# Kernel optimization log

Hardware: AMD Instinct MI355X
Metric: run time of the kernel (lower is better)

## Reference

```python
import math
import jax, jax.numpy as jnp
import numpy as np

EPS = 1e-8
N_ITER = 5


def _partial_ot(C, reg):
    # C: (M, N) cost matrix. Faithful to partial_optimal_transport with
    # diag-matmuls replaced by equivalent broadcast row/col scaling.
    M, N = C.shape
    a = jnp.full((M,), 1.0 / M, dtype=C.dtype)
    b = jnp.full((N,), 1.0 / N, dtype=C.dtype)
    m = jnp.minimum(a.sum(), b.sum())  # = 1.0 here
    K = jnp.exp(-C / jnp.clip(reg, EPS))
    K = K * (m / jnp.clip(K.sum(), EPS))

    def body(K, _):
        r = jnp.minimum(a / jnp.clip(K.sum(axis=1), EPS), 1.0)   # min(a/rowsum, dx)
        K1 = r[:, None] * K
        c = jnp.minimum(b / jnp.clip(K1.sum(axis=0), EPS), 1.0)  # min(b/colsum, dy)
        K2 = K1 * c[None, :]
        K = K2 * (m / jnp.clip(K2.sum(), EPS))
        return K, None

    K, _ = jax.lax.scan(body, K, None, length=N_ITER)
    return K


def _rigid_transform(a, b, w):
    # a: (M,3) source points, b: (M,3) weighted targets, w: (M,) weights
    wn = w[:, None] / (w.sum() + 1e-6)            # normalized weights (M,1)
    centroid_a = (a * wn).sum(axis=0)             # (3,)
    centroid_b = (b * wn).sum(axis=0)
    ac = a - centroid_a
    bc = b - centroid_b
    cov = ac.T @ (bc * wn)                        # (3,3)
    u, s, vh = jnp.linalg.svd(cov, full_matrices=False)
    v = vh.T                                      # torch.svd's V
    rot_pos = v @ u.T
    v_neg = v.at[:, 2].multiply(-1.0)
    rot_neg = v_neg @ u.T
    det = jnp.linalg.det(rot_pos)
    rot = jnp.where(det > 0, rot_pos, rot_neg)
    trans = -rot @ centroid_a + centroid_b        # (3,)
    return jnp.concatenate([rot, trans[:, None]], axis=1)  # (3,4)


def _one_sample(se, te, s, t, rho):
    # se: (D,M) src feats, te: (D,N) tgt feats, s: (3,M), t: (3,N)
    D = se.shape[0]
    scores = (se.T @ te) / math.sqrt(D)           # (M,N)
    C = -jax.nn.log_softmax(scores, axis=1)
    matches = _partial_ot(C, rho)                 # (M,N)
    rowsum = matches.sum(axis=1, keepdims=True)   # (M,1)
    weighted_ref = (matches @ t.T) / (rowsum + 1e-6)  # (M,3)
    T = _rigid_transform(s.T, weighted_ref, rowsum[:, 0])
    return T, matches


def _forward(src_embedding, tgt_embedding, src, tgt, rho):
    Ts, match_mats = jax.vmap(_one_sample, in_axes=(0, 0, 0, 0, None))(
        src_embedding, tgt_embedding, src, tgt, rho)
    return Ts[:, :3, :3], Ts[:, :3, 3], match_mats


def setup_inputs() -> dict:
    key = jax.random.key(0)
    k1, k2, k3, k4 = jax.random.split(key, 4)
    B, D, M, N = 16, 256, 2048, 2048
    return {
        "src_embedding": jax.random.normal(k1, (B, D, M), dtype=jnp.float32),
        "tgt_embedding": jax.random.normal(k2, (B, D, N), dtype=jnp.float32),
        "src": jax.random.normal(k3, (B, 3, M), dtype=jnp.float32),
        "tgt": jax.random.normal(k4, (B, 3, N), dtype=jnp.float32),
        "rho": jnp.asarray(1.0, dtype=jnp.float32),
    }


def reference(src_embedding, tgt_embedding, src, tgt, rho):
    return _forward(src_embedding, tgt_embedding, src, tgt, rho)
```

## Files before the change

### kernel.cpp

```cpp
#include <hip/hip_runtime.h>
#include <math.h>

#define B_ 16
#define D_ 256
#define M_ 2048
#define N_ 2048
#define EPSF 1e-8f
#define AVAL (1.0f/2048.0f)

typedef __bf16  bf16x8 __attribute__((ext_vector_type(8)));
typedef float   f32x4  __attribute__((ext_vector_type(4)));

__device__ __forceinline__ float wredsum(float x){
  #pragma unroll
  for (int off=32; off; off>>=1) x += __shfl_xor(x, off);
  return x;
}
__device__ __forceinline__ float wredmax(float x){
  #pragma unroll
  for (int off=32; off; off>>=1) x = fmaxf(x, __shfl_xor(x, off));
  return x;
}
__device__ __forceinline__ unsigned short f2bf(float x){
  unsigned int v = __float_as_uint(x);
  unsigned int r = (v + 0x7fffu + ((v>>16)&1u)) >> 16;
  return (unsigned short)r;
}
__device__ __forceinline__ float bf2f(unsigned short u){ return __uint_as_float(((unsigned int)u)<<16); }
__device__ __forceinline__ float h2f(unsigned short h){
  _Float16 x; __builtin_memcpy(&x,&h,2); return (float)x;
}
__device__ __forceinline__ unsigned short f2h(float x){
  _Float16 h = (_Float16)x; unsigned short u; __builtin_memcpy(&u,&h,2); return u;
}

__global__ __launch_bounds__(256) void gemm_kernel(const float* __restrict__ se,
                                                   const float* __restrict__ te,
                                                   float* __restrict__ S)
{
  __shared__ unsigned int Ah[2048], Al[2048], Bh[2048], Bl[2048];
  const int b  = blockIdx.z;
  const int mb = blockIdx.y;
  const int nb = blockIdx.x;
  const int t    = threadIdx.x;
  const int wave = t >> 6, lane = t & 63;
  const int wy = wave >> 1, wx = wave & 1;
  const int quad = lane >> 4, l15 = lane & 15;
  const int ml  = t & 127;
  const int dh  = t >> 7;

  f32x4 acc[4][4] = {};

  const float* Abase = se + (size_t)b*D_*M_ + mb*128 + ml;
  const float* Bbase = te + (size_t)b*D_*M_ + nb*128 + ml;

  for (int kc=0; kc<8; kc++){
    __syncthreads();
    {
      float x[16];
      #pragma unroll
      for (int j=0;j<16;j++) x[j] = Abase[(size_t)(kc*32 + dh*16 + j)*M_];
      #pragma unroll
      for (int gi=0; gi<2; gi++){
        unsigned int hw[4], lw[4];
        #pragma unroll
        for (int p=0;p<4;p++){
          float a0 = x[gi*8+2*p], a1 = x[gi*8+2*p+1];
          unsigned short h0 = f2bf(a0), h1 = f2bf(a1);
          unsigned short q0 = f2bf(a0 - bf2f(h0)), q1 = f2bf(a1 - bf2f(h1));
          hw[p] = (unsigned)h0 | ((unsigned)h1<<16);
          lw[p] = (unsigned)q0 | ((unsigned)q1<<16);
        }
        int idx = ((dh*2+gi)*128 + ml)*4;
        *(uint4*)&Ah[idx] = *(uint4*)hw;
        *(uint4*)&Al[idx] = *(uint4*)lw;
      }
    }
    {
      float x[16];
      #pragma unroll
      for (int j=0;j<16;j++) x[j] = Bbase[(size_t)(kc*32 + dh*16 + j)*M_];
      #pragma unroll
      for (int gi=0; gi<2; gi++){
        unsigned int hw[4], lw[4];
        #pragma unroll
        for (int p=0;p<4;p++){
          float a0 = x[gi*8+2*p], a1 = x[gi*8+2*p+1];
          unsigned short h0 = f2bf(a0), h1 = f2bf(a1);
          unsigned short q0 = f2bf(a0 - bf2f(h0)), q1 = f2bf(a1 - bf2f(h1));
          hw[p] = (unsigned)h0 | ((unsigned)h1<<16);
          lw[p] = (unsigned)q0 | ((unsigned)q1<<16);
        }
        int idx = ((dh*2+gi)*128 + ml)*4;
        *(uint4*)&Bh[idx] = *(uint4*)hw;
        *(uint4*)&Bl[idx] = *(uint4*)lw;
      }
    }
    __syncthreads();
    bf16x8 ah[4], al[4], bh[4], bl[4];
    #pragma unroll
    for (int rt=0;rt<4;rt++){
      int ra = (quad*128 + wy*64 + rt*16 + l15)*4;
      int rb = (quad*128 + wx*64 + rt*16 + l15)*4;
      ah[rt] = *(const bf16x8*)&Ah[ra];
      al[rt] = *(const bf16x8*)&Al[ra];
      bh[rt] = *(const bf16x8*)&Bh[rb];
      bl[rt] = *(const bf16x8*)&Bl[rb];
    }
    #pragma unroll
    for (int rt=0;rt<4;rt++)
      #pragma unroll
      for (int ct=0;ct<4;ct++){
        acc[rt][ct] = __builtin_amdgcn_mfma_f32_16x16x32_bf16(ah[rt], bh[ct], acc[rt][ct], 0,0,0);
        acc[rt][ct] = __builtin_amdgcn_mfma_f32_16x16x32_bf16(ah[rt], bl[ct], acc[rt][ct], 0,0,0);
        acc[rt][ct] = __builtin_amdgcn_mfma_f32_16x16x32_bf16(al[rt], bh[ct], acc[rt][ct], 0,0,0);
      }
  }
  const float sc = 0.0625f;
  #pragma unroll
  for (int rt=0;rt<4;rt++){
    #pragma unroll
    for (int r=0;r<4;r++){
      int m = mb*128 + wy*64 + rt*16 + quad*4 + r;
      float* rowp = S + (size_t)(b*M_ + m)*N_;
      #pragma unroll
      for (int ct=0;ct<4;ct++){
        int n = nb*128 + wx*64 + ct*16 + l15;
        rowp[n] = acc[rt][ct][r] * sc;
      }
    }
  }
}

__global__ __launch_bounds__(256) void stats_kernel(float* __restrict__ S,
                                                    const float* __restrict__ rho,
                                                    float* __restrict__ lse,
                                                    float* __restrict__ y0)
{
  const int b = blockIdx.y;
  const int m = blockIdx.x*4 + (threadIdx.x>>6);
  const int lane = threadIdx.x & 63;
  const float invrho = 1.0f / fmaxf(rho[0], EPSF);
  float* row = S + (size_t)(b*M_ + m)*N_;
  const float4* row4 = (const float4*)row;
  float4 vals[8];
  float mx = -3.4e38f;
  #pragma unroll
  for (int k=0;k<8;k++){
    float4 v = row4[lane + 64*k];
    vals[k] = v;
    mx = fmaxf(mx, fmaxf(fmaxf(v.x,v.y), fmaxf(v.z,v.w)));
  }
  mx = wredmax(mx);
  float e1=0.0f;
  #pragma unroll
  for (int k=0;k<8;k++){
    float4 v = vals[k];
    e1 += __expf(v.x-mx)+__expf(v.y-mx)+__expf(v.z-mx)+__expf(v.w-mx);
  }
  e1 = wredsum(e1);
  const float l = mx + __logf(e1);
  uint2* rowh2 = (uint2*)row;
  float y2 = 0.0f;
  #pragma unroll
  for (int k=0;k<8;k++){
    float4 v = vals[k];
    unsigned short h0 = f2h(__expf((v.x-l)*invrho));
    unsigned short h1 = f2h(__expf((v.y-l)*invrho));
    unsigned short h2 = f2h(__expf((v.z-l)*invrho));
    unsigned short h3 = f2h(__expf((v.w-l)*invrho));
    y2 += h2f(h0)+h2f(h1)+h2f(h2)+h2f(h3);
    uint2 pk;
    pk.x = (unsigned)h0 | ((unsigned)h1<<16);
    pk.y = (unsigned)h2 | ((unsigned)h3<<16);
    rowh2[lane + 64*k] = pk;
  }
  y2 = wredsum(y2);
  if (lane==0){
    lse[b*M_+m] = l;
    y0 [b*M_+m] = y2;
  }
}

__global__ __launch_bounds__(256) void init_kernel(const float* __restrict__ y0,
                                                   float* __restrict__ u, float* __restrict__ v,
                                                   float* __restrict__ w, float* __restrict__ g)
{
  const int b = blockIdx.x; const int t = threadIdx.x;
  float s = 0.0f;
  for (int i=t;i<M_;i+=256) s += y0[b*M_+i];
  s = wredsum(s);
  __shared__ float red[4];
  __shared__ float gsh;
  if ((t&63)==0) red[t>>6]=s;
  __syncthreads();
  if (t==0){
    float tot = red[0]+red[1]+red[2]+red[3];
    float gg = 1.0f / fmaxf(tot, EPSF);
    g[b]=gg; gsh=gg;
  }
  __syncthreads();
  float gg = gsh;
  for (int i=t;i<M_;i+=256){
    float rs = gg * y0[b*M_+i];
    u[b*M_+i] = fminf(AVAL / fmaxf(rs, EPSF), 1.0f);
    v[b*M_+i] = 1.0f;
    w[b*M_+i] = 0.0f;
  }
}

__global__ __launch_bounds__(256) void row_kernel(const float* __restrict__ S,
                                                  const float* __restrict__ vv,
                                                  float* __restrict__ u,
                                                  const float* __restrict__ g)
{
  const int b = blockIdx.y;
  const int m = blockIdx.x*4 + (threadIdx.x>>6);
  const int lane = threadIdx.x & 63;
  const uint4*  rowh = (const uint4*)(S + (size_t)(b*M_ + m)*N_);
  const float4* vp   = (const float4*)(vv + (size_t)b*N_);
  float acc=0.0f;
  #pragma unroll
  for (int k=0;k<4;k++){
    uint4 su = rowh[lane + 64*k];
    float4 v0 = vp[(lane+64*k)*2];
    float4 v1 = vp[(lane+64*k)*2+1];
    acc += h2f((unsigned short)(su.x&0xffff))*v0.x + h2f((unsigned short)(su.x>>16))*v0.y
         + h2f((unsigned short)(su.y&0xffff))*v0.z + h2f((unsigned short)(su.y>>16))*v0.w
         + h2f((unsigned short)(su.z&0xffff))*v1.x + h2f((unsigned short)(su.z>>16))*v1.y
         + h2f((unsigned short)(su.w&0xffff))*v1.z + h2f((unsigned short)(su.w>>16))*v1.w;
  }
  acc = wredsum(acc);
  if (lane==0){
    float ui = u[b*M_+m];
    float rs = g[b]*ui*acc;
    u[b*M_+m] = ui * fminf(AVAL / fmaxf(rs, EPSF), 1.0f);
  }
}

__global__ __launch_bounds__(256) void col_kernel(const float* __restrict__ S,
                                                  const float* __restrict__ u,
                                                  float* __restrict__ w)
{
  const int b  = blockIdx.y;
  const int i0 = blockIdx.x*64;
  const int t  = threadIdx.x;
  float acc[8];
  #pragma unroll
  for (int k=0;k<8;k++) acc[k]=0.0f;
  for (int i=0;i<64;i++){
    int r = i0+i;
    float ui = u[b*M_+r];
    uint4 su = ((const uint4*)(S + (size_t)(b*M_ + r)*N_))[t];
    acc[0] += ui*h2f((unsigned short)(su.x&0xffff));
    acc[1] += ui*h2f((unsigned short)(su.x>>16));
    acc[2] += ui*h2f((unsigned short)(su.y&0xffff));
    acc[3] += ui*h2f((unsigned short)(su.y>>16));
    acc[4] += ui*h2f((unsigned short)(su.z&0xffff));
    acc[5] += ui*h2f((unsigned short)(su.z>>16));
    acc[6] += ui*h2f((unsigned short)(su.w&0xffff));
    acc[7] += ui*h2f((unsigned short)(su.w>>16));
  }
  #pragma unroll
  for (int k=0;k<8;k++) atomicAdd(&w[b*N_+t*8+k], acc[k]);
}

__global__ __launch_bounds__(256) void vupd_kernel(float* __restrict__ w,
                                                   float* __restrict__ v,
                                                   float* __restrict__ g)
{
  const int b = blockIdx.x; const int t = threadIdx.x;
  const float gg = g[b];
  float part = 0.0f;
  for (int i=t;i<N_;i+=256){
    float wj = w[b*N_+i];
    float vj = v[b*N_+i];
    float c  = fminf(AVAL/fmaxf(gg*vj*wj,EPSF), 1.0f);
    vj *= c;
    v[b*N_+i]=vj;
    part += wj*vj;
    w[b*N_+i]=0.0f;
  }
  part = wredsum(part);
  __shared__ float red[4];
  if ((t&63)==0) red[t>>6]=part;
  __syncthreads();
  if (t==0){
    float tot = gg*(red[0]+red[1]+red[2]+red[3]);
    g[b] = gg / fmaxf(tot, EPSF);
  }
}

__global__ __launch_bounds__(256) void final_kernel(float* __restrict__ S,
                                                    const float* __restrict__ u,
                                                    const float* __restrict__ v,
                                                    const float* __restrict__ g,
                                                    const float* __restrict__ tgt,
                                                    float* __restrict__ rowsum,
                                                    float* __restrict__ wref)
{
  const int b = blockIdx.y;
  const int m = blockIdx.x*4 + (threadIdx.x>>6);
  const int lane = threadIdx.x & 63;
  const float gu = g[b]*u[b*M_+m];
  float* row = S + (size_t)(b*M_ + m)*N_;
  const uint4* rowh = (const uint4*)row;
  uint4 su[4];
  #pragma unroll
  for (int k=0;k<4;k++) su[k] = rowh[lane + 64*k];
  __builtin_amdgcn_s_waitcnt(0);
  float4* rowf = (float4*)row;
  const float4* vp = (const float4*)(v + (size_t)b*N_);
  const float4* t0 = (const float4*)(tgt + ((size_t)b*3+0)*N_);
  const float4* t1 = (const float4*)(tgt + ((size_t)b*3+1)*N_);
  const float4* t2 = (const float4*)(tgt + ((size_t)b*3+2)*N_);
  float rs=0.0f, a0=0.0f, a1=0.0f, a2=0.0f;
  #pragma unroll
  for (int k=0;k<4;k++){
    float s[8] = {h2f((unsigned short)(su[k].x&0xffff)), h2f((unsigned short)(su[k].x>>16)),
                  h2f((unsigned short)(su[k].y&0xffff)), h2f((unsigned short)(su[k].y>>16)),
                  h2f((unsigned short)(su[k].z&0xffff)), h2f((unsigned short)(su[k].z>>16)),
                  h2f((unsigned short)(su[k].w&0xffff)), h2f((unsigned short)(su[k].w>>16))};
    int i2 = (lane+64*k)*2;
    #pragma unroll
    for (int h=0;h<2;h++){
      float4 v4 = vp[i2+h];
      float4 q0 = t0[i2+h], q1 = t1[i2+h], q2 = t2[i2+h];
      float m0 = gu*s[h*4+0]*v4.x;
      float m1 = gu*s[h*4+1]*v4.y;
      float m2 = gu*s[h*4+2]*v4.z;
      float m3 = gu*s[h*4+3]*v4.w;
      rs += m0+m1+m2+m3;
      a0 += m0*q0.x + m1*q0.y + m2*q0.z + m3*q0.w;
      a1 += m0*q1.x + m1*q1.y + m2*q1.z + m3*q1.w;
      a2 += m0*q2.x + m1*q2.y + m2*q2.z + m3*q2.w;
      rowf[i2+h] = make_float4(m0,m1,m2,m3);
    }
  }
  rs = wredsum(rs); a0=wredsum(a0); a1=wredsum(a1); a2=wredsum(a2);
  if (lane==0){
    rowsum[b*M_+m] = rs;
    float inv = 1.0f/(rs+1e-6f);
    size_t o = ((size_t)b*M_+m)*3;
    wref[o]=a0*inv; wref[o+1]=a1*inv; wref[o+2]=a2*inv;
  }
}

__device__ __forceinline__ void mat3_svd_rot(const float cov[3][3], float R[3][3])
{
  float mx = 1e-30f;
  for (int p=0;p<3;p++) for (int q=0;q<3;q++) mx = fmaxf(mx, fabsf(cov[p][q]));
  const float inv = 1.0f/mx;
  float Cm[3][3];
  for (int p=0;p<3;p++) for (int q=0;q<3;q++) Cm[p][q]=cov[p][q]*inv;
  float G[3][3];
  for (int p=0;p<3;p++)
    for (int q=0;q<3;q++)
      G[p][q] = Cm[0][p]*Cm[0][q] + Cm[1][p]*Cm[1][q] + Cm[2][p]*Cm[2][q];
  float V[3][3] = {{1,0,0},{0,1,0},{0,0,1}};
  const int PP[3]={0,0,1}, QQ[3]={1,2,2};
  for (int sweep=0;sweep<12;sweep++){
    for (int r=0;r<3;r++){
      int p=PP[r], q=QQ[r];
      float apq = G[p][q];
      if (fabsf(apq) < 1e-20f) continue;
      float tau = (G[q][q]-G[p][p])/(2.0f*apq);
      float tt  = (tau>=0.0f?1.0f:-1.0f)/(fabsf(tau)+sqrtf(1.0f+tau*tau));
      float cc  = 1.0f/sqrtf(1.0f+tt*tt);
      float ss  = tt*cc;
      for (int k=0;k<3;k++){ float gkp=G[k][p], gkq=G[k][q]; G[k][p]=cc*gkp-ss*gkq; G[k][q]=ss*gkp+cc*gkq; }
      for (int k=0;k<3;k++){ float gpk=G[p][k], gqk=G[q][k]; G[p][k]=cc*gpk-ss*gqk; G[q][k]=ss*gpk+cc*gqk; }
      for (int k=0;k<3;k++){ float vkp=V[k][p], vkq=V[k][q]; V[k][p]=cc*vkp-ss*vkq; V[k][q]=ss*vkp+cc*vkq; }
    }
  }
  float ev[3]={G[0][0],G[1][1],G[2][2]};
  int i0=0,i1=1,i2=2,tmp;
  if (ev[i0]<ev[i1]){tmp=i0;i0=i1;i1=tmp;}
  if (ev[i0]<ev[i2]){tmp=i0;i0=i2;i2=tmp;}
  if (ev[i1]<ev[i2]){tmp=i1;i1=i2;i2=tmp;}
  const int idx[3]={i0,i1,i2};
  float Vs[3][3];
  for (int k=0;k<3;k++) for (int i=0;i<3;i++) Vs[i][k]=V[i][idx[k]];
  float U[3][3]; float nrm[3];
  for (int k=0;k<3;k++){
    float ux = Cm[0][0]*Vs[0][k]+Cm[0][1]*Vs[1][k]+Cm[0][2]*Vs[2][k];
    float uy = Cm[1][0]*Vs[0][k]+Cm[1][1]*Vs[1][k]+Cm[1][2]*Vs[2][k];
    float uz = Cm[2][0]*Vs[0][k]+Cm[2][1]*Vs[1][k]+Cm[2][2]*Vs[2][k];
    float n = sqrtf(ux*ux+uy*uy+uz*uz);
    nrm[k]=n;
    float in = (n>1e-20f)?1.0f/n:0.0f;
    U[0][k]=ux*in; U[1][k]=uy*in; U[2][k]=uz*in;
  }
  if (nrm[2] < 1e-6f*fmaxf(nrm[0],1e-20f)){
    U[0][2]=U[1][0]*U[2][1]-U[2][0]*U[1][1];
    U[1][2]=U[2][0]*U[0][1]-U[0][0]*U[2][1];
    U[2][2]=U[0][0]*U[1][1]-U[1][0]*U[0][1];
  }
  float detC = Cm[0][0]*(Cm[1][1]*Cm[2][2]-Cm[1][2]*Cm[2][1])
             - Cm[0][1]*(Cm[1][0]*Cm[2][2]-Cm[1][2]*Cm[2][0])
             + Cm[0][2]*(Cm[1][0]*Cm[2][1]-Cm[1][1]*Cm[2][0]);
  float d2 = (detC>0.0f)?1.0f:-1.0f;
  for (int p=0;p<3;p++)
    for (int q=0;q<3;q++)
      R[p][q] = Vs[p][0]*U[q][0] + Vs[p][1]*U[q][1] + d2*Vs[p][2]*U[q][2];
}

__global__ __launch_bounds__(256) void rigid_kernel(const float* __restrict__ src,
                                                    const float* __restrict__ wref,
                                                    const float* __restrict__ rowsum,
                                                    float* __restrict__ out)
{
  const int b = blockIdx.x; const int t = threadIdx.x;
  float acc[16];
  #pragma unroll
  for (int k=0;k<16;k++) acc[k]=0.0f;
  for (int i=t;i<M_;i+=256){
    float wgt = rowsum[b*M_+i];
    float ax = src[((size_t)b*3+0)*M_+i];
    float ay = src[((size_t)b*3+1)*M_+i];
    float az = src[((size_t)b*3+2)*M_+i];
    const float* wr = wref + ((size_t)b*M_+i)*3;
    float bx=wr[0], by=wr[1], bz=wr[2];
    acc[0]+=wgt;
    acc[1]+=wgt*ax; acc[2]+=wgt*ay; acc[3]+=wgt*az;
    acc[4]+=wgt*bx; acc[5]+=wgt*by; acc[6]+=wgt*bz;
    acc[7] +=wgt*ax*bx; acc[8] +=wgt*ax*by; acc[9] +=wgt*ax*bz;
    acc[10]+=wgt*ay*bx; acc[11]+=wgt*ay*by; acc[12]+=wgt*ay*bz;
    acc[13]+=wgt*az*bx; acc[14]+=wgt*az*by; acc[15]+=wgt*az*bz;
  }
  __shared__ float red[4][16];
  const int wid = t>>6, lane = t&63;
  #pragma unroll
  for (int k=0;k<16;k++){
    float v = acc[k];
    #pragma unroll
    for (int off=32; off; off>>=1) v += __shfl_xor(v, off);
    if (lane==0) red[wid][k]=v;
  }
  __syncthreads();
  if (t==0){
    float s[16];
    #pragma unroll
    for (int k=0;k<16;k++) s[k]=red[0][k]+red[1][k]+red[2][k]+red[3][k];
    float wsum = s[0];
    float denom = wsum + 1e-6f;
    float ca[3]={s[1]/denom, s[2]/denom, s[3]/denom};
    float cb[3]={s[4]/denom, s[5]/denom, s[6]/denom};
    float sw = wsum/denom;
    float cov[3][3];
    for (int p=0;p<3;p++)
      for (int q=0;q<3;q++)
        cov[p][q] = s[7+p*3+q]/denom + (sw-2.0f)*ca[p]*cb[q];
    float R[3][3];
    mat3_svd_rot(cov, R);
    float tr[3];
    for (int p=0;p<3;p++)
      tr[p] = -(R[p][0]*ca[0]+R[p][1]*ca[1]+R[p][2]*ca[2]) + cb[p];
    for (int p=0;p<3;p++)
      for (int q=0;q<3;q++)
        out[b*9 + p*3 + q] = R[p][q];
    for (int p=0;p<3;p++)
      out[144 + b*3 + p] = tr[p];
  }
}

extern "C" void kernel_launch(void* const* d_in, const int* in_sizes, int n_in,
                              void* d_out, int out_size, void* d_ws, size_t ws_size,
                              hipStream_t stream)
{
  const float* se  = (const float*)d_in[0];
  const float* te  = (const float*)d_in[1];
  const float* src = (const float*)d_in[2];
  const float* tgt = (const float*)d_in[3];
  const float* rho = (const float*)d_in[4];
  float* out = (float*)d_out;
  float* S   = out + 192;
  float* ws  = (float*)d_ws;
  float* lse = ws;
  float* y0  = ws + 32768;
  float* u   = ws + 65536;
  float* v   = ws + 98304;
  float* w   = ws + 131072;
  float* g   = ws + 163840;
  float* wref= ws + 163904;

  gemm_kernel <<<dim3(16,16,16),256,0,stream>>>(se,te,S);
  stats_kernel<<<dim3(512,16),  256,0,stream>>>(S,rho,lse,y0);
  init_kernel <<<dim3(16),      256,0,stream>>>(y0,u,v,w,g);
  for (int it=0; it<5; ++it){
    if (it>0) row_kernel<<<dim3(512,16),256,0,stream>>>(S,v,u,g);
    col_kernel <<<dim3(32,16),256,0,stream>>>(S,u,w);
    vupd_kernel<<<dim3(16),   256,0,stream>>>(w,v,g);
  }
  final_kernel<<<dim3(512,16),256,0,stream>>>(S,u,v,g,tgt,y0,wref);
  rigid_kernel<<<dim3(16),    256,0,stream>>>(src,wref,y0,out);
}
```

Baseline: 978.6 us.

## Pre-split fp32 embeddings into bf16 hi/lo planes and load via global_load_lds

Adds a conversion kernel that splits the fp32 embeddings once into packed bf16 high and low planes in workspace, arranged so each 16-byte chunk holds eight K values. A new GEMM then streams these planes directly into LDS with global_load_lds, dropping the per-tile fp32 load and bf16 split that the old GEMM repeated for every output tile. This costs an extra pass and roughly 67 MB of workspace writes and reads. The path runs only when the workspace is large enough; otherwise the old GEMM is used.

Result: faster. 923.0 us (-5.7%).

```diff
diff --git a/kernel.cpp b/kernel.cpp
--- a/kernel.cpp
+++ b/kernel.cpp
@@ -32,6 +32,109 @@
 }
 __device__ __forceinline__ unsigned short f2h(float x){
   _Float16 h = (_Float16)x; unsigned short u; __builtin_memcpy(&u,&h,2); return u;
+}
+
+__device__ __forceinline__ void gll16(const void* gsrc, void* ldst){
+  __builtin_amdgcn_global_load_lds(
+      (const __attribute__((address_space(1))) unsigned int*)gsrc,
+      (__attribute__((address_space(3))) unsigned int*)(unsigned int)(unsigned long long)ldst,
+      16, 0, 0);
+}
+
+__global__ __launch_bounds__(256) void convert_kernel(const float* __restrict__ se,
+                                                      const float* __restrict__ te,
+                                                      uint4* __restrict__ Ah, uint4* __restrict__ Al,
+                                                      uint4* __restrict__ Bh, uint4* __restrict__ Bl)
+{
+  const int t  = threadIdx.x;
+  const int mb = blockIdx.x;
+  const int g  = blockIdx.y;
+  const int z  = blockIdx.z;
+  const int b  = z & 15, op = z >> 4;
+  const int m  = mb*256 + t;
+  const float* src = (op ? te : se) + (size_t)b*D_*M_ + (size_t)g*8*M_ + m;
+  float x[8];
+  #pragma unroll
+  for (int j=0;j<8;j++) x[j] = src[(size_t)j*M_];
+  unsigned int hw[4], lw[4];
+  #pragma unroll
+  for (int p=0;p<4;p++){
+    float a0 = x[2*p], a1 = x[2*p+1];
+    unsigned short h0 = f2bf(a0), h1 = f2bf(a1);
+    unsigned short q0 = f2bf(a0 - bf2f(h0)), q1 = f2bf(a1 - bf2f(h1));
+    hw[p] = (unsigned)h0 | ((unsigned)h1<<16);
+    lw[p] = (unsigned)q0 | ((unsigned)q1<<16);
+  }
+  const size_t gi = (size_t)(b*32 + g)*2048 + m;
+  uint4* Ph = op ? Bh : Ah;
+  uint4* Pl = op ? Bl : Al;
+  Ph[gi] = *(const uint4*)hw;
+  Pl[gi] = *(const uint4*)lw;
+}
+
+__global__ __launch_bounds__(256) void gemm_fast(const uint4* __restrict__ Ah,
+                                                 const uint4* __restrict__ Al,
+                                                 const uint4* __restrict__ Bh,
+                                                 const uint4* __restrict__ Bl,
+                                                 float* __restrict__ S)
+{
+  __shared__ unsigned int sAh[2048], sAl[2048], sBh[2048], sBl[2048];
+  const int b  = blockIdx.z;
+  const int mb = blockIdx.y;
+  const int nb = blockIdx.x;
+  const int t    = threadIdx.x;
+  const int wave = t >> 6, lane = t & 63;
+  const int wy = wave >> 1, wx = wave & 1;
+  const int quad = lane >> 4, l15 = lane & 15;
+
+  f32x4 acc[4][4] = {};
+
+  for (int kc=0; kc<8; kc++){
+    __syncthreads();
+    #pragma unroll
+    for (int r=0;r<2;r++){
+      const int i  = r*256 + t;
+      const int gq = i >> 7, m = i & 127;
+      const size_t rowg = (size_t)(b*32 + kc*4 + gq)*2048;
+      gll16(Ah + rowg + mb*128 + m, (char*)sAh + (size_t)i*16);
+      gll16(Al + rowg + mb*128 + m, (char*)sAl + (size_t)i*16);
+      gll16(Bh + rowg + nb*128 + m, (char*)sBh + (size_t)i*16);
+      gll16(Bl + rowg + nb*128 + m, (char*)sBl + (size_t)i*16);
+    }
+    __syncthreads();
+    bf16x8 ah[4], al[4], bh[4], bl[4];
+    #pragma unroll
+    for (int rt=0;rt<4;rt++){
+      int ra = (quad*128 + wy*64 + rt*16 + l15)*4;
+      int rb = (quad*128 + wx*64 + rt*16 + l15)*4;
+      ah[rt] = *(const bf16x8*)&sAh[ra];
+      al[rt] = *(const bf16x8*)&sAl[ra];
+      bh[rt] = *(const bf16x8*)&sBh[rb];
+      bl[rt] = *(const bf16x8*)&sBl[rb];
+    }
+    #pragma unroll
+    for (int rt=0;rt<4;rt++)
+      #pragma unroll
+      for (int ct=0;ct<4;ct++){
+        acc[rt][ct] = __builtin_amdgcn_mfma_f32_16x16x32_bf16(ah[rt], bh[ct], acc[rt][ct], 0,0,0);
+        acc[rt][ct] = __builtin_amdgcn_mfma_f32_16x16x32_bf16(ah[rt], bl[ct], acc[rt][ct], 0,0,0);
+        acc[rt][ct] = __builtin_amdgcn_mfma_f32_16x16x32_bf16(al[rt], bh[ct], acc[rt][ct], 0,0,0);
+      }
+  }
+  const float sc = 0.0625f;
+  #pragma unroll
+  for (int rt=0;rt<4;rt++){
+    #pragma unroll
+    for (int r=0;r<4;r++){
+      int m = mb*128 + wy*64 + rt*16 + quad*4 + r;
+      float* rowp = S + (size_t)(b*M_ + m)*N_;
+      #pragma unroll
+      for (int ct=0;ct<4;ct++){
+        int n = nb*128 + wx*64 + ct*16 + l15;
+        rowp[n] = acc[rt][ct][r] * sc;
+      }
+    }
+  }
 }
 
 __global__ __launch_bounds__(256) void gemm_kernel(const float* __restrict__ se,
@@ -484,7 +587,21 @@
   float* g   = ws + 163840;
   float* wref= ws + 163904;
 
-  gemm_kernel <<<dim3(16,16,16),256,0,stream>>>(se,te,S);
+  const size_t PLANE_G     = (size_t)16*32*2048;
+  const size_t PLANE_BYTES = PLANE_G*16;
+  const size_t PLANE_OFF   = 1048832;
+  const size_t need        = PLANE_OFF + 4*PLANE_BYTES;
+
+  if (ws_size >= need){
+    uint4* Ah = (uint4*)((char*)d_ws + PLANE_OFF);
+    uint4* Al = Ah + PLANE_G;
+    uint4* Bh = Al + PLANE_G;
+    uint4* Bl = Bh + PLANE_G;
+    convert_kernel<<<dim3(8,32,32),256,0,stream>>>(se,te,Ah,Al,Bh,Bl);
+    gemm_fast     <<<dim3(16,16,16),256,0,stream>>>(Ah,Al,Bh,Bl,S);
+  } else {
+    gemm_kernel   <<<dim3(16,16,16),256,0,stream>>>(se,te,S);
+  }
   stats_kernel<<<dim3(512,16),  256,0,stream>>>(S,rho,lse,y0);
   init_kernel <<<dim3(16),      256,0,stream>>>(y0,u,v,w,g);
   for (int it=0; it<5; ++it){
```
